# Kernel optimization log

Hardware: AMD Instinct MI355X
Metric: run time of the kernel (lower is better)

The kernel has to match this reference:

```python
import jax, jax.numpy as jnp
import numpy as np

N = 6144
INPUT_SIZE = 1024
HIDDEN = 256
NEG_INF = -9e15  # matches torch masked_fill value -9000000000000000.0


def setup_inputs() -> dict:
    key = jax.random.key(0)
    k1, k2, k3, k4 = jax.random.split(key, 4)
    nodes_embed = jax.random.normal(k1, (N, INPUT_SIZE), dtype=jnp.float32)
    node_adj = jax.random.randint(k2, (N, N), 0, 2, dtype=jnp.int32)
    # learned params (xavier-uniform-ish scaling)
    limW = np.sqrt(6.0 / (INPUT_SIZE + HIDDEN))
    W = jax.random.uniform(k3, (INPUT_SIZE, HIDDEN), minval=-limW, maxval=limW, dtype=jnp.float32)
    lima = 1.414 * np.sqrt(6.0 / (2 * HIDDEN + 1))
    a_edge = jax.random.uniform(k4, (2 * HIDDEN,), minval=-lima, maxval=lima, dtype=jnp.float32)
    return {"nodes_embed": nodes_embed, "W": W, "a_edge": a_edge, "node_adj": node_adj}


def reference(nodes_embed, W, a_edge, node_adj):
    # h = nodes_embed @ W : [N, hidden]
    h = nodes_embed @ W
    # W_edge([h_i ; h_j]) decomposes exactly: (h_i @ a1) + (h_j @ a2)
    a1, a2 = a_edge[:HIDDEN], a_edge[HIDDEN:]
    score = (h @ a1)[:, None] + (h @ a2)[None, :]  # [N, N]
    adj_f = node_adj.astype(h.dtype)
    weight = jax.nn.leaky_relu(adj_f * score, negative_slope=0.2)
    weight = jnp.where(node_adj == 0, jnp.asarray(NEG_INF, h.dtype), weight)
    attention = jax.nn.softmax(weight, axis=-1)
    # dropout in eval mode (identity)
    return attention @ h  # [N, hidden]
```

## Files before the change

kernel.cpp:

```cpp
#include <hip/hip_runtime.h>
#include <hip/hip_bf16.h>

#define NN 6144
#define INPUT 1024
#define HID 256

using frag  = __attribute__((ext_vector_type(8))) short;
using f32x4 = __attribute__((ext_vector_type(4))) float;

static __device__ __forceinline__ unsigned short bf16u(float x) {
    unsigned u = __float_as_uint(x);
    u += 0x7fff + ((u >> 16) & 1);
    return (unsigned short)(u >> 16);
}

__global__ __launch_bounds__(256) void k_convert_w(const float* __restrict__ W,
                                                   unsigned short* __restrict__ Wt) {
    int t = blockIdx.x * 256 + threadIdx.x;
    int n = t >> 10, k = t & 1023;
    Wt[t] = bf16u(W[k * HID + n]);
}

__global__ __launch_bounds__(256) void k_gemm1(const float* __restrict__ X,
                                               const unsigned short* __restrict__ Wt,
                                               const float* __restrict__ a_edge,
                                               unsigned short* __restrict__ hT,
                                               float* __restrict__ s1,
                                               float* __restrict__ s2) {
    __shared__ unsigned short A[2][32][72];
    int t = threadIdx.x;
    int m = t >> 3, cg = t & 7;
    int i0 = blockIdx.x * 32, n0 = blockIdx.y * 64;
    int w = t >> 6, l = t & 63, lm = l & 15, q = l >> 4;
    int nw = n0 + w * 16;

    const float* xrow = X + (size_t)(i0 + m) * INPUT + cg * 8;
    const unsigned short* brow = Wt + (size_t)(nw + lm) * INPUT + q * 8;

    f32x4 acc0 = {}, acc1 = {};

    for (int c = 0; c < 16; c++) {
        int buf = c & 1;
        float4 xa = *reinterpret_cast<const float4*>(xrow + c * 64);
        float4 xb = *reinterpret_cast<const float4*>(xrow + c * 64 + 4);
        frag av;
        av[0] = (short)bf16u(xa.x); av[1] = (short)bf16u(xa.y);
        av[2] = (short)bf16u(xa.z); av[3] = (short)bf16u(xa.w);
        av[4] = (short)bf16u(xb.x); av[5] = (short)bf16u(xb.y);
        av[6] = (short)bf16u(xb.z); av[7] = (short)bf16u(xb.w);
        *reinterpret_cast<frag*>(&A[buf][m][cg * 8]) = av;

        __syncthreads();

#pragma unroll
        for (int kk = 0; kk < 2; kk++) {
            frag a0 = *reinterpret_cast<const frag*>(&A[buf][lm][kk * 32 + q * 8]);
            frag a1 = *reinterpret_cast<const frag*>(&A[buf][16 + lm][kk * 32 + q * 8]);
            frag b  = *reinterpret_cast<const frag*>(brow + c * 64 + kk * 32);
            acc0 = __builtin_amdgcn_mfma_f32_16x16x32_bf16(a0, b, acc0, 0, 0, 0);
            acc1 = __builtin_amdgcn_mfma_f32_16x16x32_bf16(a1, b, acc1, 0, 0, 0);
        }
    }

    ushort4 o;
    o.x = bf16u(acc0[0]); o.y = bf16u(acc0[1]); o.z = bf16u(acc0[2]); o.w = bf16u(acc0[3]);
    *reinterpret_cast<ushort4*>(hT + (size_t)(nw + lm) * NN + i0 + q * 4) = o;
    o.x = bf16u(acc1[0]); o.y = bf16u(acc1[1]); o.z = bf16u(acc1[2]); o.w = bf16u(acc1[3]);
    *reinterpret_cast<ushort4*>(hT + (size_t)(nw + lm) * NN + i0 + 16 + q * 4) = o;

    float a1v = a_edge[nw + lm], a2v = a_edge[HID + nw + lm];
#pragma unroll
    for (int h = 0; h < 2; h++) {
        const f32x4& ac = h ? acc1 : acc0;
#pragma unroll
        for (int r = 0; r < 4; r++) {
            float v1 = ac[r] * a1v, v2 = ac[r] * a2v;
            v1 += __shfl_xor(v1, 1); v2 += __shfl_xor(v2, 1);
            v1 += __shfl_xor(v1, 2); v2 += __shfl_xor(v2, 2);
            v1 += __shfl_xor(v1, 4); v2 += __shfl_xor(v2, 4);
            v1 += __shfl_xor(v1, 8); v2 += __shfl_xor(v2, 8);
            if (lm == 0) {
                atomicAdd(&s1[i0 + h * 16 + q * 4 + r], v1);
                atomicAdd(&s2[i0 + h * 16 + q * 4 + r], v2);
            }
        }
    }
}

__global__ __launch_bounds__(256) void k_attn(const int* __restrict__ adj,
                                              const float* __restrict__ s1,
                                              const float* __restrict__ s2,
                                              const unsigned short* __restrict__ hT,
                                              float* __restrict__ U4,
                                              float* __restrict__ denom4) {
    __shared__ unsigned short P[2][32][136];
    int t = threadIdx.x;
    int m = t >> 3, cg = t & 7;
    int i0 = blockIdx.x * 32;
    int q4 = blockIdx.y;
    int j0 = q4 * 1536;
    int w = t >> 6, l = t & 63, lm = l & 15, q = l >> 4;

    float s1v = s1[i0 + m];
    const int*   arow = adj + (size_t)(i0 + m) * NN + j0 + cg * 4;
    const float* s2p  = s2 + j0 + cg * 4;

    const unsigned short* brow[4];
#pragma unroll
    for (int nt = 0; nt < 4; nt++)
        brow[nt] = hT + (size_t)(w * 64 + nt * 16 + lm) * NN + j0 + q * 8;

    f32x4 acc[2][4] = {};
    float dsum = 0.f;

    for (int c = 0; c < 12; c++) {
        int buf = c & 1;
        int jc = c * 128;
#pragma unroll
        for (int p = 0; p < 4; p++) {
            int4   av = *reinterpret_cast<const int4*>(arow + jc + p * 32);
            float4 sv = *reinterpret_cast<const float4*>(s2p + jc + p * 32);
            float sc, wv, p0, p1, p2, p3;
            sc = s1v + sv.x; wv = fmaxf(sc, 0.2f * sc); p0 = av.x ? __expf(wv) : 0.f;
            sc = s1v + sv.y; wv = fmaxf(sc, 0.2f * sc); p1 = av.y ? __expf(wv) : 0.f;
            sc = s1v + sv.z; wv = fmaxf(sc, 0.2f * sc); p2 = av.z ? __expf(wv) : 0.f;
            sc = s1v + sv.w; wv = fmaxf(sc, 0.2f * sc); p3 = av.w ? __expf(wv) : 0.f;
            dsum += (p0 + p1) + (p2 + p3);
            ushort4 pk;
            pk.x = bf16u(p0); pk.y = bf16u(p1); pk.z = bf16u(p2); pk.w = bf16u(p3);
            *reinterpret_cast<ushort4*>(&P[buf][m][p * 32 + cg * 4]) = pk;
        }
        __syncthreads();
#pragma unroll
        for (int kk = 0; kk < 4; kk++) {
            frag a0 = *reinterpret_cast<const frag*>(&P[buf][lm][kk * 32 + q * 8]);
            frag a1 = *reinterpret_cast<const frag*>(&P[buf][16 + lm][kk * 32 + q * 8]);
#pragma unroll
            for (int nt = 0; nt < 4; nt++) {
                frag b = *reinterpret_cast<const frag*>(brow[nt] + jc + kk * 32);
                acc[0][nt] = __builtin_amdgcn_mfma_f32_16x16x32_bf16(a0, b, acc[0][nt], 0, 0, 0);
                acc[1][nt] = __builtin_amdgcn_mfma_f32_16x16x32_bf16(a1, b, acc[1][nt], 0, 0, 0);
            }
        }
    }

    float v = dsum;
    v += __shfl_xor(v, 1); v += __shfl_xor(v, 2); v += __shfl_xor(v, 4);
    if (cg == 0) denom4[(size_t)q4 * NN + i0 + m] = v;

    float* Ub = U4 + (size_t)q4 * NN * HID;
#pragma unroll
    for (int h = 0; h < 2; h++)
#pragma unroll
        for (int nt = 0; nt < 4; nt++)
#pragma unroll
            for (int r = 0; r < 4; r++)
                Ub[(size_t)(i0 + h * 16 + q * 4 + r) * HID + w * 64 + nt * 16 + lm] = acc[h][nt][r];
}

__global__ __launch_bounds__(256) void k_norm(const float* __restrict__ U4,
                                              const float* __restrict__ denom4,
                                              float* __restrict__ out) {
    int i = blockIdx.x, t = threadIdx.x;
    size_t S = (size_t)NN * HID;
    size_t base = (size_t)i * HID + t;
    float u = U4[base] + U4[base + S] + U4[base + 2 * S] + U4[base + 3 * S];
    float d = denom4[i] + denom4[i + NN] + denom4[i + 2 * NN] + denom4[i + 3 * NN];
    out[base] = (d != 0.f) ? u / d : 0.f;
}

extern "C" void kernel_launch(void* const* d_in, const int* in_sizes, int n_in,
                              void* d_out, int out_size, void* d_ws, size_t ws_size,
                              hipStream_t stream) {
    const float* X      = (const float*)d_in[0];
    const float* W      = (const float*)d_in[1];
    const float* a_edge = (const float*)d_in[2];
    const int*   adj    = (const int*)d_in[3];
    float* out = (float*)d_out;

    float* U4     = (float*)d_ws;
    float* denom4 = U4 + (size_t)4 * NN * HID;
    float* s1     = denom4 + (size_t)4 * NN;
    float* s2     = s1 + NN;
    unsigned short* hT = (unsigned short*)(s2 + NN);
    unsigned short* Wt = hT + (size_t)HID * NN;

    hipMemsetAsync(s1, 0, 2 * NN * sizeof(float), stream);
    k_convert_w<<<INPUT * HID / 256, 256, 0, stream>>>(W, Wt);
    k_gemm1<<<dim3(NN / 32, HID / 64), 256, 0, stream>>>(X, Wt, a_edge, hT, s1, s2);
    k_attn<<<dim3(NN / 32, 4), 256, 0, stream>>>(adj, s1, s2, hT, U4, denom4);
    k_norm<<<NN, 256, 0, stream>>>(U4, denom4, out);
}
```

Measured before the change: 307.5 us.

## Drop LDS staging and register-prefetch operands in gemm1 and attention kernels

Both GEMM kernels now build MFMA A-fragments directly in registers, with each lane computing the probabilities or bf16 conversions for its own fragment. This removes the shared-memory round trip and the __syncthreads barrier. Next-iteration global loads are software-prefetched into registers to hide latency. The attention split over the j dimension goes from 4 to 2 with 16-row tiles, which shrinks the partial U buffers and the reduction work in k_norm. The tradeoff is more register pressure, and adj rows are read as 32-byte per-lane segments spread across 16 rows, which may coalesce less well.

```diff
diff --git a/kernel.cpp b/kernel.cpp
--- a/kernel.cpp
+++ b/kernel.cpp
@@ -7,6 +7,18 @@
 
 using frag  = __attribute__((ext_vector_type(8))) short;
 using f32x4 = __attribute__((ext_vector_type(4))) float;
+
+union fragcvt { frag f; __hip_bfloat162 h[4]; };
+
+static __device__ __forceinline__ frag pack8(float p0, float p1, float p2, float p3,
+                                             float p4, float p5, float p6, float p7) {
+    fragcvt u;
+    u.h[0] = __float22bfloat162_rn(make_float2(p0, p1));
+    u.h[1] = __float22bfloat162_rn(make_float2(p2, p3));
+    u.h[2] = __float22bfloat162_rn(make_float2(p4, p5));
+    u.h[3] = __float22bfloat162_rn(make_float2(p6, p7));
+    return u.f;
+}
 
 static __device__ __forceinline__ unsigned short bf16u(float x) {
     unsigned u = __float_as_uint(x);
@@ -27,145 +39,151 @@
                                                unsigned short* __restrict__ hT,
                                                float* __restrict__ s1,
                                                float* __restrict__ s2) {
-    __shared__ unsigned short A[2][32][72];
-    int t = threadIdx.x;
-    int m = t >> 3, cg = t & 7;
-    int i0 = blockIdx.x * 32, n0 = blockIdx.y * 64;
-    int w = t >> 6, l = t & 63, lm = l & 15, q = l >> 4;
-    int nw = n0 + w * 16;
-
-    const float* xrow = X + (size_t)(i0 + m) * INPUT + cg * 8;
-    const unsigned short* brow = Wt + (size_t)(nw + lm) * INPUT + q * 8;
-
-    f32x4 acc0 = {}, acc1 = {};
-
-    for (int c = 0; c < 16; c++) {
-        int buf = c & 1;
-        float4 xa = *reinterpret_cast<const float4*>(xrow + c * 64);
-        float4 xb = *reinterpret_cast<const float4*>(xrow + c * 64 + 4);
-        frag av;
-        av[0] = (short)bf16u(xa.x); av[1] = (short)bf16u(xa.y);
-        av[2] = (short)bf16u(xa.z); av[3] = (short)bf16u(xa.w);
-        av[4] = (short)bf16u(xb.x); av[5] = (short)bf16u(xb.y);
-        av[6] = (short)bf16u(xb.z); av[7] = (short)bf16u(xb.w);
-        *reinterpret_cast<frag*>(&A[buf][m][cg * 8]) = av;
-
-        __syncthreads();
-
-#pragma unroll
-        for (int kk = 0; kk < 2; kk++) {
-            frag a0 = *reinterpret_cast<const frag*>(&A[buf][lm][kk * 32 + q * 8]);
-            frag a1 = *reinterpret_cast<const frag*>(&A[buf][16 + lm][kk * 32 + q * 8]);
-            frag b  = *reinterpret_cast<const frag*>(brow + c * 64 + kk * 32);
-            acc0 = __builtin_amdgcn_mfma_f32_16x16x32_bf16(a0, b, acc0, 0, 0, 0);
-            acc1 = __builtin_amdgcn_mfma_f32_16x16x32_bf16(a1, b, acc1, 0, 0, 0);
+    int t = threadIdx.x, w = t >> 6, l = t & 63, lm = l & 15, q = l >> 4;
+    int i0 = blockIdx.x * 16;
+    int n0 = w * 64;
+
+    const float* xp = X + (size_t)(i0 + lm) * INPUT + q * 8;
+    const unsigned short* wp = Wt + (size_t)(n0 + lm) * INPUT + q * 8;
+    const int WS = 16 * INPUT;
+
+    f32x4 acc[4] = {};
+    float4 cx0 = *reinterpret_cast<const float4*>(xp);
+    float4 cx1 = *reinterpret_cast<const float4*>(xp + 4);
+    frag cw0 = *reinterpret_cast<const frag*>(wp);
+    frag cw1 = *reinterpret_cast<const frag*>(wp + WS);
+    frag cw2 = *reinterpret_cast<const frag*>(wp + 2 * WS);
+    frag cw3 = *reinterpret_cast<const frag*>(wp + 3 * WS);
+
+#pragma unroll 2
+    for (int it = 0; it < 32; it++) {
+        int kn = ((it < 31) ? (it + 1) : it) * 32;
+        float4 nx0 = *reinterpret_cast<const float4*>(xp + kn);
+        float4 nx1 = *reinterpret_cast<const float4*>(xp + kn + 4);
+        frag nw0 = *reinterpret_cast<const frag*>(wp + kn);
+        frag nw1 = *reinterpret_cast<const frag*>(wp + WS + kn);
+        frag nw2 = *reinterpret_cast<const frag*>(wp + 2 * WS + kn);
+        frag nw3 = *reinterpret_cast<const frag*>(wp + 3 * WS + kn);
+
+        frag af = pack8(cx0.x, cx0.y, cx0.z, cx0.w, cx1.x, cx1.y, cx1.z, cx1.w);
+        acc[0] = __builtin_amdgcn_mfma_f32_16x16x32_bf16(af, cw0, acc[0], 0, 0, 0);
+        acc[1] = __builtin_amdgcn_mfma_f32_16x16x32_bf16(af, cw1, acc[1], 0, 0, 0);
+        acc[2] = __builtin_amdgcn_mfma_f32_16x16x32_bf16(af, cw2, acc[2], 0, 0, 0);
+        acc[3] = __builtin_amdgcn_mfma_f32_16x16x32_bf16(af, cw3, acc[3], 0, 0, 0);
+
+        cx0 = nx0; cx1 = nx1; cw0 = nw0; cw1 = nw1; cw2 = nw2; cw3 = nw3;
+    }
+
+#pragma unroll
+    for (int nt = 0; nt < 4; nt++) {
+        ushort4 o;
+        o.x = bf16u(acc[nt][0]); o.y = bf16u(acc[nt][1]);
+        o.z = bf16u(acc[nt][2]); o.w = bf16u(acc[nt][3]);
+        *reinterpret_cast<ushort4*>(hT + (size_t)(n0 + nt * 16 + lm) * NN + i0 + q * 4) = o;
+    }
+
+    float a1v0 = a_edge[n0 + lm],            a1v1 = a_edge[n0 + 16 + lm];
+    float a1v2 = a_edge[n0 + 32 + lm],       a1v3 = a_edge[n0 + 48 + lm];
+    float a2v0 = a_edge[HID + n0 + lm],      a2v1 = a_edge[HID + n0 + 16 + lm];
+    float a2v2 = a_edge[HID + n0 + 32 + lm], a2v3 = a_edge[HID + n0 + 48 + lm];
+#pragma unroll
+    for (int r = 0; r < 4; r++) {
+        float v1 = acc[0][r] * a1v0 + acc[1][r] * a1v1 + acc[2][r] * a1v2 + acc[3][r] * a1v3;
+        float v2 = acc[0][r] * a2v0 + acc[1][r] * a2v1 + acc[2][r] * a2v2 + acc[3][r] * a2v3;
+        v1 += __shfl_xor(v1, 1); v2 += __shfl_xor(v2, 1);
+        v1 += __shfl_xor(v1, 2); v2 += __shfl_xor(v2, 2);
+        v1 += __shfl_xor(v1, 4); v2 += __shfl_xor(v2, 4);
+        v1 += __shfl_xor(v1, 8); v2 += __shfl_xor(v2, 8);
+        if (lm == 0) {
+            atomicAdd(&s1[i0 + q * 4 + r], v1);
+            atomicAdd(&s2[i0 + q * 4 + r], v2);
         }
     }
-
-    ushort4 o;
-    o.x = bf16u(acc0[0]); o.y = bf16u(acc0[1]); o.z = bf16u(acc0[2]); o.w = bf16u(acc0[3]);
-    *reinterpret_cast<ushort4*>(hT + (size_t)(nw + lm) * NN + i0 + q * 4) = o;
-    o.x = bf16u(acc1[0]); o.y = bf16u(acc1[1]); o.z = bf16u(acc1[2]); o.w = bf16u(acc1[3]);
-    *reinterpret_cast<ushort4*>(hT + (size_t)(nw + lm) * NN + i0 + 16 + q * 4) = o;
-
-    float a1v = a_edge[nw + lm], a2v = a_edge[HID + nw + lm];
-#pragma unroll
-    for (int h = 0; h < 2; h++) {
-        const f32x4& ac = h ? acc1 : acc0;
-#pragma unroll
-        for (int r = 0; r < 4; r++) {
-            float v1 = ac[r] * a1v, v2 = ac[r] * a2v;
-            v1 += __shfl_xor(v1, 1); v2 += __shfl_xor(v2, 1);
-            v1 += __shfl_xor(v1, 2); v2 += __shfl_xor(v2, 2);
-            v1 += __shfl_xor(v1, 4); v2 += __shfl_xor(v2, 4);
-            v1 += __shfl_xor(v1, 8); v2 += __shfl_xor(v2, 8);
-            if (lm == 0) {
-                atomicAdd(&s1[i0 + h * 16 + q * 4 + r], v1);
-                atomicAdd(&s2[i0 + h * 16 + q * 4 + r], v2);
-            }
-        }
-    }
-}
-
-__global__ __launch_bounds__(256) void k_attn(const int* __restrict__ adj,
-                                              const float* __restrict__ s1,
-                                              const float* __restrict__ s2,
-                                              const unsigned short* __restrict__ hT,
-                                              float* __restrict__ U4,
-                                              float* __restrict__ denom4) {
-    __shared__ unsigned short P[2][32][136];
-    int t = threadIdx.x;
-    int m = t >> 3, cg = t & 7;
-    int i0 = blockIdx.x * 32;
-    int q4 = blockIdx.y;
-    int j0 = q4 * 1536;
-    int w = t >> 6, l = t & 63, lm = l & 15, q = l >> 4;
-
-    float s1v = s1[i0 + m];
-    const int*   arow = adj + (size_t)(i0 + m) * NN + j0 + cg * 4;
-    const float* s2p  = s2 + j0 + cg * 4;
-
-    const unsigned short* brow[4];
+}
+
+__global__ __launch_bounds__(256, 3) void k_attn(const int* __restrict__ adj,
+                                                 const float* __restrict__ s1,
+                                                 const float* __restrict__ s2,
+                                                 const unsigned short* __restrict__ hT,
+                                                 float* __restrict__ U2,
+                                                 float* __restrict__ denom2) {
+    int t = threadIdx.x, w = t >> 6, l = t & 63, lm = l & 15, q = l >> 4;
+    int i0 = blockIdx.x * 16;
+    int jh = blockIdx.y;
+    int j0 = jh * 3072;
+    int row = i0 + lm;
+
+    float s1v = s1[row];
+    const int*   ap = adj + (size_t)row * NN + j0 + q * 8;
+    const float* sp = s2 + j0 + q * 8;
+    const unsigned short* bp = hT + (size_t)(w * 64 + lm) * NN + j0 + q * 8;
+    const int BS = 16 * NN;
+
+    f32x4 acc[4] = {};
+    float dsum = 0.f;
+
+    int4   ca0 = *reinterpret_cast<const int4*>(ap);
+    int4   ca1 = *reinterpret_cast<const int4*>(ap + 4);
+    float4 cs0 = *reinterpret_cast<const float4*>(sp);
+    float4 cs1 = *reinterpret_cast<const float4*>(sp + 4);
+    frag cb0 = *reinterpret_cast<const frag*>(bp);
+    frag cb1 = *reinterpret_cast<const frag*>(bp + BS);
+    frag cb2 = *reinterpret_cast<const frag*>(bp + 2 * BS);
+    frag cb3 = *reinterpret_cast<const frag*>(bp + 3 * BS);
+
+#pragma unroll 2
+    for (int it = 0; it < 96; it++) {
+        int kn = ((it < 95) ? (it + 1) : it) * 32;
+        int4   na0 = *reinterpret_cast<const int4*>(ap + kn);
+        int4   na1 = *reinterpret_cast<const int4*>(ap + kn + 4);
+        float4 ns0 = *reinterpret_cast<const float4*>(sp + kn);
+        float4 ns1 = *reinterpret_cast<const float4*>(sp + kn + 4);
+        frag nb0 = *reinterpret_cast<const frag*>(bp + kn);
+        frag nb1 = *reinterpret_cast<const frag*>(bp + BS + kn);
+        frag nb2 = *reinterpret_cast<const frag*>(bp + 2 * BS + kn);
+        frag nb3 = *reinterpret_cast<const frag*>(bp + 3 * BS + kn);
+
+        float sc, e, p0, p1, p2, p3, p4, p5, p6, p7;
+        sc = s1v + cs0.x; e = __expf(fmaxf(sc, 0.2f * sc)); p0 = ca0.x ? e : 0.f;
+        sc = s1v + cs0.y; e = __expf(fmaxf(sc, 0.2f * sc)); p1 = ca0.y ? e : 0.f;
+        sc = s1v + cs0.z; e = __expf(fmaxf(sc, 0.2f * sc)); p2 = ca0.z ? e : 0.f;
+        sc = s1v + cs0.w; e = __expf(fmaxf(sc, 0.2f * sc)); p3 = ca0.w ? e : 0.f;
+        sc = s1v + cs1.x; e = __expf(fmaxf(sc, 0.2f * sc)); p4 = ca1.x ? e : 0.f;
+        sc = s1v + cs1.y; e = __expf(fmaxf(sc, 0.2f * sc)); p5 = ca1.y ? e : 0.f;
+        sc = s1v + cs1.z; e = __expf(fmaxf(sc, 0.2f * sc)); p6 = ca1.z ? e : 0.f;
+        sc = s1v + cs1.w; e = __expf(fmaxf(sc, 0.2f * sc)); p7 = ca1.w ? e : 0.f;
+        dsum += ((p0 + p1) + (p2 + p3)) + ((p4 + p5) + (p6 + p7));
+
+        frag af = pack8(p0, p1, p2, p3, p4, p5, p6, p7);
+        acc[0] = __builtin_amdgcn_mfma_f32_16x16x32_bf16(af, cb0, acc[0], 0, 0, 0);
+        acc[1] = __builtin_amdgcn_mfma_f32_16x16x32_bf16(af, cb1, acc[1], 0, 0, 0);
+        acc[2] = __builtin_amdgcn_mfma_f32_16x16x32_bf16(af, cb2, acc[2], 0, 0, 0);
+        acc[3] = __builtin_amdgcn_mfma_f32_16x16x32_bf16(af, cb3, acc[3], 0, 0, 0);
+
+        ca0 = na0; ca1 = na1; cs0 = ns0; cs1 = ns1;
+        cb0 = nb0; cb1 = nb1; cb2 = nb2; cb3 = nb3;
+    }
+
+    dsum += __shfl_xor(dsum, 16);
+    dsum += __shfl_xor(dsum, 32);
+    if (w == 0 && q == 0) denom2[(size_t)jh * NN + row] = dsum;
+
+    float* Ub = U2 + (size_t)jh * NN * HID;
 #pragma unroll
     for (int nt = 0; nt < 4; nt++)
-        brow[nt] = hT + (size_t)(w * 64 + nt * 16 + lm) * NN + j0 + q * 8;
-
-    f32x4 acc[2][4] = {};
-    float dsum = 0.f;
-
-    for (int c = 0; c < 12; c++) {
-        int buf = c & 1;
-        int jc = c * 128;
-#pragma unroll
-        for (int p = 0; p < 4; p++) {
-            int4   av = *reinterpret_cast<const int4*>(arow + jc + p * 32);
-            float4 sv = *reinterpret_cast<const float4*>(s2p + jc + p * 32);
-            float sc, wv, p0, p1, p2, p3;
-            sc = s1v + sv.x; wv = fmaxf(sc, 0.2f * sc); p0 = av.x ? __expf(wv) : 0.f;
-            sc = s1v + sv.y; wv = fmaxf(sc, 0.2f * sc); p1 = av.y ? __expf(wv) : 0.f;
-            sc = s1v + sv.z; wv = fmaxf(sc, 0.2f * sc); p2 = av.z ? __expf(wv) : 0.f;
-            sc = s1v + sv.w; wv = fmaxf(sc, 0.2f * sc); p3 = av.w ? __expf(wv) : 0.f;
-            dsum += (p0 + p1) + (p2 + p3);
-            ushort4 pk;
-            pk.x = bf16u(p0); pk.y = bf16u(p1); pk.z = bf16u(p2); pk.w = bf16u(p3);
-            *reinterpret_cast<ushort4*>(&P[buf][m][p * 32 + cg * 4]) = pk;
-        }
-        __syncthreads();
-#pragma unroll
-        for (int kk = 0; kk < 4; kk++) {
-            frag a0 = *reinterpret_cast<const frag*>(&P[buf][lm][kk * 32 + q * 8]);
-            frag a1 = *reinterpret_cast<const frag*>(&P[buf][16 + lm][kk * 32 + q * 8]);
-#pragma unroll
-            for (int nt = 0; nt < 4; nt++) {
-                frag b = *reinterpret_cast<const frag*>(brow[nt] + jc + kk * 32);
-                acc[0][nt] = __builtin_amdgcn_mfma_f32_16x16x32_bf16(a0, b, acc[0][nt], 0, 0, 0);
-                acc[1][nt] = __builtin_amdgcn_mfma_f32_16x16x32_bf16(a1, b, acc[1][nt], 0, 0, 0);
-            }
-        }
-    }
-
-    float v = dsum;
-    v += __shfl_xor(v, 1); v += __shfl_xor(v, 2); v += __shfl_xor(v, 4);
-    if (cg == 0) denom4[(size_t)q4 * NN + i0 + m] = v;
-
-    float* Ub = U4 + (size_t)q4 * NN * HID;
-#pragma unroll
-    for (int h = 0; h < 2; h++)
-#pragma unroll
-        for (int nt = 0; nt < 4; nt++)
-#pragma unroll
-            for (int r = 0; r < 4; r++)
-                Ub[(size_t)(i0 + h * 16 + q * 4 + r) * HID + w * 64 + nt * 16 + lm] = acc[h][nt][r];
-}
-
-__global__ __launch_bounds__(256) void k_norm(const float* __restrict__ U4,
-                                              const float* __restrict__ denom4,
+#pragma unroll
+        for (int r = 0; r < 4; r++)
+            Ub[(size_t)(i0 + q * 4 + r) * HID + w * 64 + nt * 16 + lm] = acc[nt][r];
+}
+
+__global__ __launch_bounds__(256) void k_norm(const float* __restrict__ U2,
+                                              const float* __restrict__ denom2,
                                               float* __restrict__ out) {
     int i = blockIdx.x, t = threadIdx.x;
     size_t S = (size_t)NN * HID;
     size_t base = (size_t)i * HID + t;
-    float u = U4[base] + U4[base + S] + U4[base + 2 * S] + U4[base + 3 * S];
-    float d = denom4[i] + denom4[i + NN] + denom4[i + 2 * NN] + denom4[i + 3 * NN];
+    float u = U2[base] + U2[base + S];
+    float d = denom2[i] + denom2[i + NN];
     out[base] = (d != 0.f) ? u / d : 0.f;
 }
 
@@ -178,16 +196,16 @@
     const int*   adj    = (const int*)d_in[3];
     float* out = (float*)d_out;
 
-    float* U4     = (float*)d_ws;
-    float* denom4 = U4 + (size_t)4 * NN * HID;
-    float* s1     = denom4 + (size_t)4 * NN;
+    float* U2     = (float*)d_ws;
+    float* denom2 = U2 + (size_t)2 * NN * HID;
+    float* s1     = denom2 + 2 * NN;
     float* s2     = s1 + NN;
     unsigned short* hT = (unsigned short*)(s2 + NN);
     unsigned short* Wt = hT + (size_t)HID * NN;
 
     hipMemsetAsync(s1, 0, 2 * NN * sizeof(float), stream);
     k_convert_w<<<INPUT * HID / 256, 256, 0, stream>>>(W, Wt);
-    k_gemm1<<<dim3(NN / 32, HID / 64), 256, 0, stream>>>(X, Wt, a_edge, hT, s1, s2);
-    k_attn<<<dim3(NN / 32, 4), 256, 0, stream>>>(adj, s1, s2, hT, U4, denom4);
-    k_norm<<<NN, 256, 0, stream>>>(U4, denom4, out);
-}
+    k_gemm1<<<NN / 16, 256, 0, stream>>>(X, Wt, a_edge, hT, s1, s2);
+    k_attn<<<dim3(NN / 16, 2), 256, 0, stream>>>(adj, s1, s2, hT, U2, denom2);
+    k_norm<<<NN, 256, 0, stream>>>(U2, denom2, out);
+}
```

Result: slower. 471.7 us (+53.4%).

## Compute attention probabilities directly in MFMA fragment layout and split columns eightfold

Applied to the files above, without the earlier changes.

The attention kernel now has each thread compute the exp-probabilities for exactly the 8 elements it will feed as an MFMA A-fragment. It packs them with bf16x2 conversion and stores them in a fragment-ordered LDS layout, so the reads are simple and conflict-free. The column dimension is split into 8 partitions when the workspace is large enough, giving more blocks and better occupancy (launch bounds 256,5). The cost is larger partial-sum buffers and more reduction traffic in the normalization kernel.

```diff
diff --git a/kernel.cpp b/kernel.cpp
--- a/kernel.cpp
+++ b/kernel.cpp
@@ -7,6 +7,18 @@
 
 using frag  = __attribute__((ext_vector_type(8))) short;
 using f32x4 = __attribute__((ext_vector_type(4))) float;
+
+union fragcvt { frag f; __hip_bfloat162 h[4]; };
+
+static __device__ __forceinline__ frag pack8(float p0, float p1, float p2, float p3,
+                                             float p4, float p5, float p6, float p7) {
+    fragcvt u;
+    u.h[0] = __float22bfloat162_rn(make_float2(p0, p1));
+    u.h[1] = __float22bfloat162_rn(make_float2(p2, p3));
+    u.h[2] = __float22bfloat162_rn(make_float2(p4, p5));
+    u.h[3] = __float22bfloat162_rn(make_float2(p6, p7));
+    return u.f;
+}
 
 static __device__ __forceinline__ unsigned short bf16u(float x) {
     unsigned u = __float_as_uint(x);
@@ -87,85 +99,112 @@
     }
 }
 
-__global__ __launch_bounds__(256) void k_attn(const int* __restrict__ adj,
-                                              const float* __restrict__ s1,
-                                              const float* __restrict__ s2,
-                                              const unsigned short* __restrict__ hT,
-                                              float* __restrict__ U4,
-                                              float* __restrict__ denom4) {
-    __shared__ unsigned short P[2][32][136];
+__global__ __launch_bounds__(256, 5) void k_attn(const int* __restrict__ adj,
+                                                 const float* __restrict__ s1,
+                                                 const float* __restrict__ s2,
+                                                 const unsigned short* __restrict__ hT,
+                                                 float* __restrict__ Up,
+                                                 float* __restrict__ denomp,
+                                                 int colsPer) {
+    __shared__ unsigned short PF[2][4][2][64][8];
+    __shared__ float dred[4][32];
+
     int t = threadIdx.x;
-    int m = t >> 3, cg = t & 7;
+    int w = t >> 6, l = t & 63, lm = l & 15, q = l >> 4;
     int i0 = blockIdx.x * 32;
-    int q4 = blockIdx.y;
-    int j0 = q4 * 1536;
-    int w = t >> 6, l = t & 63, lm = l & 15, q = l >> 4;
-
-    float s1v = s1[i0 + m];
-    const int*   arow = adj + (size_t)(i0 + m) * NN + j0 + cg * 4;
-    const float* s2p  = s2 + j0 + cg * 4;
-
-    const unsigned short* brow[4];
-#pragma unroll
-    for (int nt = 0; nt < 4; nt++)
-        brow[nt] = hT + (size_t)(w * 64 + nt * 16 + lm) * NN + j0 + q * 8;
+    int jh = blockIdx.y;
+    int j0 = jh * colsPer;
+    int nchunk = colsPer >> 7;
+    int r0 = i0 + lm, r1 = r0 + 16;
+
+    float s1v0 = s1[r0], s1v1 = s1[r1];
+    const int*   ap0 = adj + (size_t)r0 * NN + j0 + w * 32 + q * 8;
+    const int*   ap1 = adj + (size_t)r1 * NN + j0 + w * 32 + q * 8;
+    const float* sp  = s2 + j0 + w * 32 + q * 8;
+    const unsigned short* bp = hT + (size_t)(w * 64 + lm) * NN + j0 + q * 8;
 
     f32x4 acc[2][4] = {};
-    float dsum = 0.f;
-
-    for (int c = 0; c < 12; c++) {
-        int buf = c & 1;
-        int jc = c * 128;
-#pragma unroll
-        for (int p = 0; p < 4; p++) {
-            int4   av = *reinterpret_cast<const int4*>(arow + jc + p * 32);
-            float4 sv = *reinterpret_cast<const float4*>(s2p + jc + p * 32);
-            float sc, wv, p0, p1, p2, p3;
-            sc = s1v + sv.x; wv = fmaxf(sc, 0.2f * sc); p0 = av.x ? __expf(wv) : 0.f;
-            sc = s1v + sv.y; wv = fmaxf(sc, 0.2f * sc); p1 = av.y ? __expf(wv) : 0.f;
-            sc = s1v + sv.z; wv = fmaxf(sc, 0.2f * sc); p2 = av.z ? __expf(wv) : 0.f;
-            sc = s1v + sv.w; wv = fmaxf(sc, 0.2f * sc); p3 = av.w ? __expf(wv) : 0.f;
-            dsum += (p0 + p1) + (p2 + p3);
-            ushort4 pk;
-            pk.x = bf16u(p0); pk.y = bf16u(p1); pk.z = bf16u(p2); pk.w = bf16u(p3);
-            *reinterpret_cast<ushort4*>(&P[buf][m][p * 32 + cg * 4]) = pk;
-        }
+    float d0 = 0.f, d1 = 0.f;
+
+    for (int c = 0; c < nchunk; c++) {
+        int buf = c & 1, jc = c * 128;
+        int4   a00 = *reinterpret_cast<const int4*>(ap0 + jc);
+        int4   a01 = *reinterpret_cast<const int4*>(ap0 + jc + 4);
+        int4   a10 = *reinterpret_cast<const int4*>(ap1 + jc);
+        int4   a11 = *reinterpret_cast<const int4*>(ap1 + jc + 4);
+        float4 sv0 = *reinterpret_cast<const float4*>(sp + jc);
+        float4 sv1 = *reinterpret_cast<const float4*>(sp + jc + 4);
+
+        float sc, e;
+        float p0, p1, p2, p3, p4, p5, p6, p7;
+        sc = s1v0 + sv0.x; e = __expf(fmaxf(sc, 0.2f * sc)); p0 = a00.x ? e : 0.f;
+        sc = s1v0 + sv0.y; e = __expf(fmaxf(sc, 0.2f * sc)); p1 = a00.y ? e : 0.f;
+        sc = s1v0 + sv0.z; e = __expf(fmaxf(sc, 0.2f * sc)); p2 = a00.z ? e : 0.f;
+        sc = s1v0 + sv0.w; e = __expf(fmaxf(sc, 0.2f * sc)); p3 = a00.w ? e : 0.f;
+        sc = s1v0 + sv1.x; e = __expf(fmaxf(sc, 0.2f * sc)); p4 = a01.x ? e : 0.f;
+        sc = s1v0 + sv1.y; e = __expf(fmaxf(sc, 0.2f * sc)); p5 = a01.y ? e : 0.f;
+        sc = s1v0 + sv1.z; e = __expf(fmaxf(sc, 0.2f * sc)); p6 = a01.z ? e : 0.f;
+        sc = s1v0 + sv1.w; e = __expf(fmaxf(sc, 0.2f * sc)); p7 = a01.w ? e : 0.f;
+        d0 += ((p0 + p1) + (p2 + p3)) + ((p4 + p5) + (p6 + p7));
+        frag af0 = pack8(p0, p1, p2, p3, p4, p5, p6, p7);
+        sc = s1v1 + sv0.x; e = __expf(fmaxf(sc, 0.2f * sc)); p0 = a10.x ? e : 0.f;
+        sc = s1v1 + sv0.y; e = __expf(fmaxf(sc, 0.2f * sc)); p1 = a10.y ? e : 0.f;
+        sc = s1v1 + sv0.z; e = __expf(fmaxf(sc, 0.2f * sc)); p2 = a10.z ? e : 0.f;
+        sc = s1v1 + sv0.w; e = __expf(fmaxf(sc, 0.2f * sc)); p3 = a10.w ? e : 0.f;
+        sc = s1v1 + sv1.x; e = __expf(fmaxf(sc, 0.2f * sc)); p4 = a11.x ? e : 0.f;
+        sc = s1v1 + sv1.y; e = __expf(fmaxf(sc, 0.2f * sc)); p5 = a11.y ? e : 0.f;
+        sc = s1v1 + sv1.z; e = __expf(fmaxf(sc, 0.2f * sc)); p6 = a11.z ? e : 0.f;
+        sc = s1v1 + sv1.w; e = __expf(fmaxf(sc, 0.2f * sc)); p7 = a11.w ? e : 0.f;
+        d1 += ((p0 + p1) + (p2 + p3)) + ((p4 + p5) + (p6 + p7));
+        frag af1 = pack8(p0, p1, p2, p3, p4, p5, p6, p7);
+
+        *reinterpret_cast<frag*>(&PF[buf][w][0][l][0]) = af0;
+        *reinterpret_cast<frag*>(&PF[buf][w][1][l][0]) = af1;
+
         __syncthreads();
+
 #pragma unroll
         for (int kk = 0; kk < 4; kk++) {
-            frag a0 = *reinterpret_cast<const frag*>(&P[buf][lm][kk * 32 + q * 8]);
-            frag a1 = *reinterpret_cast<const frag*>(&P[buf][16 + lm][kk * 32 + q * 8]);
+            frag a0 = *reinterpret_cast<const frag*>(&PF[buf][kk][0][l][0]);
+            frag a1 = *reinterpret_cast<const frag*>(&PF[buf][kk][1][l][0]);
+            const unsigned short* bb = bp + jc + kk * 32;
 #pragma unroll
             for (int nt = 0; nt < 4; nt++) {
-                frag b = *reinterpret_cast<const frag*>(brow[nt] + jc + kk * 32);
+                frag b = *reinterpret_cast<const frag*>(bb + nt * 16 * NN);
                 acc[0][nt] = __builtin_amdgcn_mfma_f32_16x16x32_bf16(a0, b, acc[0][nt], 0, 0, 0);
                 acc[1][nt] = __builtin_amdgcn_mfma_f32_16x16x32_bf16(a1, b, acc[1][nt], 0, 0, 0);
             }
         }
     }
 
-    float v = dsum;
-    v += __shfl_xor(v, 1); v += __shfl_xor(v, 2); v += __shfl_xor(v, 4);
-    if (cg == 0) denom4[(size_t)q4 * NN + i0 + m] = v;
-
-    float* Ub = U4 + (size_t)q4 * NN * HID;
-#pragma unroll
-    for (int h = 0; h < 2; h++)
+    d0 += __shfl_xor(d0, 16); d0 += __shfl_xor(d0, 32);
+    d1 += __shfl_xor(d1, 16); d1 += __shfl_xor(d1, 32);
+    if (q == 0) { dred[w][lm] = d0; dred[w][16 + lm] = d1; }
+    __syncthreads();
+    if (t < 32)
+        denomp[(size_t)jh * NN + i0 + t] = dred[0][t] + dred[1][t] + dred[2][t] + dred[3][t];
+
+    float* Ub = Up + (size_t)jh * NN * HID;
+#pragma unroll
+    for (int f = 0; f < 2; f++)
 #pragma unroll
         for (int nt = 0; nt < 4; nt++)
 #pragma unroll
             for (int r = 0; r < 4; r++)
-                Ub[(size_t)(i0 + h * 16 + q * 4 + r) * HID + w * 64 + nt * 16 + lm] = acc[h][nt][r];
-}
-
-__global__ __launch_bounds__(256) void k_norm(const float* __restrict__ U4,
-                                              const float* __restrict__ denom4,
-                                              float* __restrict__ out) {
+                Ub[(size_t)(i0 + f * 16 + q * 4 + r) * HID + w * 64 + nt * 16 + lm] = acc[f][nt][r];
+}
+
+__global__ __launch_bounds__(256) void k_norm(const float* __restrict__ Up,
+                                              const float* __restrict__ denomp,
+                                              float* __restrict__ out, int nj) {
     int i = blockIdx.x, t = threadIdx.x;
     size_t S = (size_t)NN * HID;
     size_t base = (size_t)i * HID + t;
-    float u = U4[base] + U4[base + S] + U4[base + 2 * S] + U4[base + 3 * S];
-    float d = denom4[i] + denom4[i + NN] + denom4[i + 2 * NN] + denom4[i + 3 * NN];
+    float u = 0.f, d = 0.f;
+    for (int j = 0; j < nj; j++) {
+        u += Up[base + (size_t)j * S];
+        d += denomp[i + (size_t)j * NN];
+    }
     out[base] = (d != 0.f) ? u / d : 0.f;
 }
 
@@ -178,9 +217,16 @@
     const int*   adj    = (const int*)d_in[3];
     float* out = (float*)d_out;
 
-    float* U4     = (float*)d_ws;
-    float* denom4 = U4 + (size_t)4 * NN * HID;
-    float* s1     = denom4 + (size_t)4 * NN;
+    auto need = [](int nj) -> size_t {
+        return (size_t)4 * ((size_t)nj * NN * HID + (size_t)nj * NN + 2 * NN)
+             + (size_t)2 * ((size_t)HID * NN + (size_t)HID * INPUT);
+    };
+    int nj = (ws_size >= need(8)) ? 8 : 4;
+    int colsPer = NN / nj;
+
+    float* Up     = (float*)d_ws;
+    float* denomp = Up + (size_t)nj * NN * HID;
+    float* s1     = denomp + (size_t)nj * NN;
     float* s2     = s1 + NN;
     unsigned short* hT = (unsigned short*)(s2 + NN);
     unsigned short* Wt = hT + (size_t)HID * NN;
@@ -188,6 +234,6 @@
     hipMemsetAsync(s1, 0, 2 * NN * sizeof(float), stream);
     k_convert_w<<<INPUT * HID / 256, 256, 0, stream>>>(W, Wt);
     k_gemm1<<<dim3(NN / 32, HID / 64), 256, 0, stream>>>(X, Wt, a_edge, hT, s1, s2);
-    k_attn<<<dim3(NN / 32, 4), 256, 0, stream>>>(adj, s1, s2, hT, U4, denom4);
-    k_norm<<<NN, 256, 0, stream>>>(U4, denom4, out);
-}
+    k_attn<<<dim3(NN / 32, nj), 256, 0, stream>>>(adj, s1, s2, hT, Up, denomp, colsPer);
+    k_norm<<<NN, 256, 0, stream>>>(Up, denomp, out, nj);
+}
```

After: 357.9 us. 1.16x slower.
